# Kernel optimization log

Hardware: AMD Instinct MI355X
Metric: run time of the kernel (lower is better)

The kernel has to match this reference:

```python
import jax, jax.numpy as jnp
import numpy as np

N_NODES = 100000
N_EDGES = 800000
IN_DIM, HID_DIM, OUT_DIM = 128, 64, 7


def setup_inputs() -> dict:
    key = jax.random.key(0)
    ks = jax.random.split(key, 8)
    x = jax.random.normal(ks[0], (N_NODES, IN_DIM), dtype=jnp.float32)
    edge_index = jax.random.randint(ks[1], (2, N_EDGES), 0, N_NODES, dtype=jnp.int64)
    # Glorot-ish init for weights, zeros for bias (PyG GCNConv default)
    def glorot(k, shape):
        lim = float(np.sqrt(6.0 / (shape[0] + shape[1])))
        return jax.random.uniform(k, shape, dtype=jnp.float32, minval=-lim, maxval=lim)
    return {
        "x": x,
        "edge_index": edge_index,
        "W1": glorot(ks[2], (IN_DIM, HID_DIM)),
        "b1": jnp.zeros((HID_DIM,), jnp.float32),
        "W2": glorot(ks[3], (HID_DIM, HID_DIM)),
        "b2": jnp.zeros((HID_DIM,), jnp.float32),
        "W3": glorot(ks[4], (HID_DIM, OUT_DIM)),
        "b3": jnp.zeros((OUT_DIM,), jnp.float32),
    }


def _gcn_conv(h_in, src, dst, W, b, n_nodes):
    # PyG GCNConv: h = x @ W; add self-loops; D^-1/2 A_hat D^-1/2 aggregation; + b
    h = h_in @ W  # [N, F_out]
    # degree over destination nodes, +1 for self-loop
    deg = jax.ops.segment_sum(jnp.ones_like(dst, dtype=h.dtype), dst,
                              num_segments=n_nodes) + 1.0
    dinv = jax.lax.rsqrt(deg)  # [N]
    coef = dinv[src] * dinv[dst]  # [E]
    msg = h[src] * coef[:, None]  # gather + scale  [E, F_out]
    out = jax.ops.segment_sum(msg, dst, num_segments=n_nodes)  # scatter-add
    out = out + h * (dinv * dinv)[:, None]  # self-loop contribution
    return out + b


def reference(x, edge_index, W1, b1, W2, b2, W3, b3):
    src, dst = edge_index[0], edge_index[1]
    n = x.shape[0]
    h = jax.nn.relu(_gcn_conv(x, src, dst, W1, b1, n))
    # dropout(p=0.5) is identity in eval mode
    h = jax.nn.relu(_gcn_conv(h, src, dst, W2, b2, n))
    return _gcn_conv(h, src, dst, W3, b3, n)
```

## Files before the change

kernel.cpp:

```cpp
#include <hip/hip_runtime.h>

#define N_NODES 100000
#define N_EDGES 800000
#define IN_DIM 128
#define HID 64
#define OUT_DIM 7
#define CAP 32
#define NGROUP 4
#define DSLICE (N_NODES / NGROUP)
#define SUBBLK 780
#define NB_N ((N_NODES + 255) / 256)

typedef __bf16 vbf8 __attribute__((ext_vector_type(8)));
typedef float  vf4  __attribute__((ext_vector_type(4)));

__device__ __forceinline__ void wswz_body(int idx, const float* __restrict__ W,
                                          __bf16* __restrict__ out) {
    int j  = idx & 7;
    int l  = (idx >> 3) & 63;
    int nt = (idx >> 9) & 3;
    int ks = idx >> 11;
    int k  = ks * 32 + ((l >> 4) << 3) + j;
    int n  = nt * 16 + (l & 15);
    out[idx] = (__bf16)W[k * 64 + n];
}

__global__ __launch_bounds__(256)
void k_init(const float* __restrict__ W1, __bf16* __restrict__ Wz1,
            const float* __restrict__ W2, __bf16* __restrict__ Wz2) {
    int b = blockIdx.x;
    if (b < 32) wswz_body(b * 256 + threadIdx.x, W1, Wz1);
    else        wswz_body((b - 32) * 256 + threadIdx.x, W2, Wz2);
}

template<int K, bool F32IN>
__device__ __forceinline__ void gemm_mfma_body(int g, int tid,
                                               const void* __restrict__ Xv,
                                               const __bf16* __restrict__ Wswz,
                                               __bf16* __restrict__ Hb) {
    constexpr int KS = K / 32;
    const int lane = tid & 63;
    const int w = g * 4 + (tid >> 6);
    if (w >= N_NODES / 16) return;
    const int r0 = w * 16;
    const int m = lane & 15;
    const int quad = lane >> 4;

    vbf8 bfrag[KS][4];
    const vbf8* wp = (const vbf8*)Wswz;
    #pragma unroll
    for (int ks = 0; ks < KS; ++ks)
        #pragma unroll
        for (int nt = 0; nt < 4; ++nt)
            bfrag[ks][nt] = wp[(ks * 4 + nt) * 64 + lane];

    vf4 acc[4] = {};
    #pragma unroll
    for (int ks = 0; ks < KS; ++ks) {
        vbf8 a;
        if (F32IN) {
            const float* xp = (const float*)Xv + (size_t)(r0 + m) * K + ks * 32 + quad * 8;
            float4 f0 = *(const float4*)xp;
            float4 f1 = *(const float4*)(xp + 4);
            a[0] = (__bf16)f0.x; a[1] = (__bf16)f0.y; a[2] = (__bf16)f0.z; a[3] = (__bf16)f0.w;
            a[4] = (__bf16)f1.x; a[5] = (__bf16)f1.y; a[6] = (__bf16)f1.z; a[7] = (__bf16)f1.w;
        } else {
            a = *(const vbf8*)((const __bf16*)Xv + (size_t)(r0 + m) * K + ks * 32 + quad * 8);
        }
        #pragma unroll
        for (int nt = 0; nt < 4; ++nt)
            acc[nt] = __builtin_amdgcn_mfma_f32_16x16x32_bf16(a, bfrag[ks][nt], acc[nt], 0, 0, 0);
    }
    #pragma unroll
    for (int nt = 0; nt < 4; ++nt)
        #pragma unroll
        for (int r = 0; r < 4; ++r)
            Hb[(size_t)(r0 + quad * 4 + r) * 64 + nt * 16 + m] = (__bf16)acc[nt][r];
}

#define FILL_BLKS (NGROUP * SUBBLK)
#define GEMM_BLKS ((N_NODES / 16 + 3) / 4)
__global__ __launch_bounds__(256)
void k_build_gemm1(const int* __restrict__ ei, int* __restrict__ cnt,
                   int* __restrict__ csr, const float* __restrict__ X,
                   const __bf16* __restrict__ Wz1, __bf16* __restrict__ Hb) {
    int b = blockIdx.x;
    if (b < GEMM_BLKS) {
        gemm_mfma_body<IN_DIM, true>(b, threadIdx.x, X, Wz1, Hb);
    } else {
        int bb = b - GEMM_BLKS;
        int group = bb & 3, sub = bb >> 2;
        int lo = group * DSLICE;
        const int4* dst4 = (const int4*)(ei + N_EDGES);
        const int4* src4 = (const int4*)ei;
        for (int e4 = sub * 256 + threadIdx.x; e4 < N_EDGES / 4; e4 += SUBBLK * 256) {
            int4 d4 = dst4[e4];
            int4 s4 = src4[e4];
            bool m0 = (unsigned)(d4.x - lo) < (unsigned)DSLICE;
            bool m1 = (unsigned)(d4.y - lo) < (unsigned)DSLICE;
            bool m2 = (unsigned)(d4.z - lo) < (unsigned)DSLICE;
            bool m3 = (unsigned)(d4.w - lo) < (unsigned)DSLICE;
            if (!(m0 | m1 | m2 | m3)) continue;
            if (m0) { int p = atomicAdd(&cnt[d4.x], 1); if (p < CAP) csr[(size_t)d4.x * CAP + p] = s4.x; }
            if (m1) { int p = atomicAdd(&cnt[d4.y], 1); if (p < CAP) csr[(size_t)d4.y * CAP + p] = s4.y; }
            if (m2) { int p = atomicAdd(&cnt[d4.z], 1); if (p < CAP) csr[(size_t)d4.z * CAP + p] = s4.z; }
            if (m3) { int p = atomicAdd(&cnt[d4.w], 1); if (p < CAP) csr[(size_t)d4.w * CAP + p] = s4.w; }
        }
    }
}

__global__ __launch_bounds__(256)
void k_gemm2(const __bf16* __restrict__ Ab, const __bf16* __restrict__ Wz2,
             __bf16* __restrict__ Hb) {
    gemm_mfma_body<HID, false>(blockIdx.x, threadIdx.x, Ab, Wz2, Hb);
}

__global__ __launch_bounds__(256)
void k_gather64(const int* __restrict__ cnt, const int* __restrict__ csr,
                const float* __restrict__ bias, const __bf16* __restrict__ Hb,
                __bf16* __restrict__ Ab) {
    int node = blockIdx.x * 32 + (threadIdx.x >> 3);
    int q = threadIdx.x & 7;
    if (node >= N_NODES) return;
    int deg = cnt[node];
    int end = deg < CAP ? deg : CAP;
    float dd = rsqrtf((float)deg + 1.0f);
    float d2 = dd * dd;
    vbf8 h8 = *(const vbf8*)(Hb + (size_t)node * 64 + q * 8);
    float4 b0 = *(const float4*)(bias + q * 8);
    float4 b1 = *(const float4*)(bias + q * 8 + 4);
    float acc[8];
    acc[0] = fmaf((float)h8[0], d2, b0.x); acc[1] = fmaf((float)h8[1], d2, b0.y);
    acc[2] = fmaf((float)h8[2], d2, b0.z); acc[3] = fmaf((float)h8[3], d2, b0.w);
    acc[4] = fmaf((float)h8[4], d2, b1.x); acc[5] = fmaf((float)h8[5], d2, b1.y);
    acc[6] = fmaf((float)h8[6], d2, b1.z); acc[7] = fmaf((float)h8[7], d2, b1.w);

    const int4* row4 = (const int4*)(csr + (size_t)node * CAP);
    int4 qa = row4[0], qb = row4[1], qc = row4[2], qd = row4[3];
    int srcs[16] = {qa.x, qa.y, qa.z, qa.w, qb.x, qb.y, qb.z, qb.w,
                    qc.x, qc.y, qc.z, qc.w, qd.x, qd.y, qd.z, qd.w};
    #pragma unroll
    for (int t = 0; t < 16; ++t) {
        bool live = t < end;
        int s = live ? srcs[t] : node;
        int cs = cnt[s];
        vbf8 v = *(const vbf8*)(Hb + (size_t)s * 64 + q * 8);
        float c = live ? rsqrtf((float)cs + 1.0f) * dd : 0.0f;
        #pragma unroll
        for (int u = 0; u < 8; ++u) acc[u] = fmaf((float)v[u], c, acc[u]);
    }
    for (int j = 16; j < end; ++j) {
        int s = (csr + (size_t)node * CAP)[j];
        float c = rsqrtf((float)cnt[s] + 1.0f) * dd;
        vbf8 v = *(const vbf8*)(Hb + (size_t)s * 64 + q * 8);
        #pragma unroll
        for (int u = 0; u < 8; ++u) acc[u] = fmaf((float)v[u], c, acc[u]);
    }
    vbf8 o;
    #pragma unroll
    for (int t = 0; t < 8; ++t) o[t] = (__bf16)fmaxf(acc[t], 0.f);
    *(vbf8*)(Ab + (size_t)node * 64 + q * 8) = o;
}

__global__ __launch_bounds__(256)
void k_gather64m(const int* __restrict__ cnt, const int* __restrict__ csr,
                 const float* __restrict__ bias, const __bf16* __restrict__ Hb,
                 const float* __restrict__ W3, float* __restrict__ S) {
    int node = blockIdx.x * 32 + (threadIdx.x >> 3);
    int q = threadIdx.x & 7;
    if (node >= N_NODES) return;
    int deg = cnt[node];
    int end = deg < CAP ? deg : CAP;
    float dd = rsqrtf((float)deg + 1.0f);
    float d2 = dd * dd;
    vbf8 h8 = *(const vbf8*)(Hb + (size_t)node * 64 + q * 8);
    float4 b0 = *(const float4*)(bias + q * 8);
    float4 b1 = *(const float4*)(bias + q * 8 + 4);
    float acc[8];
    acc[0] = fmaf((float)h8[0], d2, b0.x); acc[1] = fmaf((float)h8[1], d2, b0.y);
    acc[2] = fmaf((float)h8[2], d2, b0.z); acc[3] = fmaf((float)h8[3], d2, b0.w);
    acc[4] = fmaf((float)h8[4], d2, b1.x); acc[5] = fmaf((float)h8[5], d2, b1.y);
    acc[6] = fmaf((float)h8[6], d2, b1.z); acc[7] = fmaf((float)h8[7], d2, b1.w);

    const int4* row4 = (const int4*)(csr + (size_t)node * CAP);
    int4 qa = row4[0], qb = row4[1], qc = row4[2], qd = row4[3];
    int srcs[16] = {qa.x, qa.y, qa.z, qa.w, qb.x, qb.y, qb.z, qb.w,
                    qc.x, qc.y, qc.z, qc.w, qd.x, qd.y, qd.z, qd.w};
    #pragma unroll
    for (int t = 0; t < 16; ++t) {
        bool live = t < end;
        int s = live ? srcs[t] : node;
        int cs = cnt[s];
        vbf8 v = *(const vbf8*)(Hb + (size_t)s * 64 + q * 8);
        float c = live ? rsqrtf((float)cs + 1.0f) * dd : 0.0f;
        #pragma unroll
        for (int u = 0; u < 8; ++u) acc[u] = fmaf((float)v[u], c, acc[u]);
    }
    for (int j = 16; j < end; ++j) {
        int s = (csr + (size_t)node * CAP)[j];
        float c = rsqrtf((float)cnt[s] + 1.0f) * dd;
        vbf8 v = *(const vbf8*)(Hb + (size_t)s * 64 + q * 8);
        #pragma unroll
        for (int u = 0; u < 8; ++u) acc[u] = fmaf((float)v[u], c, acc[u]);
    }

    float p[7] = {};
    #pragma unroll
    for (int t = 0; t < 8; ++t) {
        float r = fmaxf(acc[t], 0.f);
        #pragma unroll
        for (int j = 0; j < 7; ++j)
            p[j] = fmaf(r, W3[(q * 8 + t) * 7 + j], p[j]);
    }
    #pragma unroll
    for (int msk = 1; msk < 8; msk <<= 1)
        #pragma unroll
        for (int j = 0; j < 7; ++j)
            p[j] += __shfl_xor(p[j], msk, 8);
    if (q < 7) {
        float v = p[0];
        if (q == 1) v = p[1]; else if (q == 2) v = p[2]; else if (q == 3) v = p[3];
        else if (q == 4) v = p[4]; else if (q == 5) v = p[5]; else if (q == 6) v = p[6];
        S[(size_t)node * 7 + q] = v;
    }
}

__global__ __launch_bounds__(256)
void k_gather7(const int* __restrict__ cnt, const int* __restrict__ csr,
               const float* __restrict__ S, const float* __restrict__ b3,
               float* __restrict__ Out) {
    int node = blockIdx.x * 32 + (threadIdx.x >> 3);
    int j7 = threadIdx.x & 7;
    if (node >= N_NODES || j7 >= 7) return;
    int deg = cnt[node];
    int end = deg < CAP ? deg : CAP;
    float dd = rsqrtf((float)deg + 1.0f);
    float d2 = dd * dd;
    const int4* row4 = (const int4*)(csr + (size_t)node * CAP);
    int4 qa = row4[0], qb = row4[1], qc = row4[2], qd = row4[3];
    int srcs[16] = {qa.x, qa.y, qa.z, qa.w, qb.x, qb.y, qb.z, qb.w,
                    qc.x, qc.y, qc.z, qc.w, qd.x, qd.y, qd.z, qd.w};
    float acc = fmaf(S[(size_t)node * 7 + j7], d2, b3[j7]);
    #pragma unroll
    for (int t = 0; t < 16; ++t) {
        bool live = t < end;
        int s = live ? srcs[t] : node;
        int cs = cnt[s];
        float v = S[(size_t)s * 7 + j7];
        float c = live ? rsqrtf((float)cs + 1.0f) * dd : 0.0f;
        acc = fmaf(v, c, acc);
    }
    for (int j = 16; j < end; ++j) {
        int s = (csr + (size_t)node * CAP)[j];
        float c = rsqrtf((float)cnt[s] + 1.0f) * dd;
        acc = fmaf(S[(size_t)s * 7 + j7], c, acc);
    }
    Out[(size_t)node * 7 + j7] = acc;
}

static inline size_t align256(size_t x) { return (x + 255) & ~(size_t)255; }

extern "C" void kernel_launch(void* const* d_in, const int* in_sizes, int n_in,
                              void* d_out, int out_size, void* d_ws, size_t ws_size,
                              hipStream_t stream) {
    const float* x  = (const float*)d_in[0];
    const int*   ei = (const int*)d_in[1];
    const float* W1 = (const float*)d_in[2];
    const float* b1 = (const float*)d_in[3];
    const float* W2 = (const float*)d_in[4];
    const float* b2 = (const float*)d_in[5];
    const float* W3 = (const float*)d_in[6];
    const float* b3 = (const float*)d_in[7];
    float* out = (float*)d_out;

    char* wsp = (char*)d_ws;
    int*    cnt  = (int*)wsp;    wsp += align256(sizeof(int) * N_NODES);
    int*    csr  = (int*)wsp;    wsp += align256(sizeof(int) * (size_t)N_NODES * CAP);
    __bf16* Wz1  = (__bf16*)wsp; wsp += align256(sizeof(__bf16) * IN_DIM * 64);
    __bf16* Wz2  = (__bf16*)wsp; wsp += align256(sizeof(__bf16) * HID * 64);
    __bf16* HbA  = (__bf16*)wsp; wsp += align256(sizeof(__bf16) * (size_t)N_NODES * 64);
    __bf16* Ab   = (__bf16*)wsp; wsp += align256(sizeof(__bf16) * (size_t)N_NODES * 64);
    __bf16* HbB  = (__bf16*)wsp; wsp += align256(sizeof(__bf16) * (size_t)N_NODES * 64);
    float*  bufS = (float*)wsp;  wsp += align256(sizeof(float) * (size_t)N_NODES * 7);

    hipMemsetAsync(cnt, 0, sizeof(int) * N_NODES, stream);
    k_init<<<48, 256, 0, stream>>>(W1, Wz1, W2, Wz2);
    k_build_gemm1<<<GEMM_BLKS + FILL_BLKS, 256, 0, stream>>>(ei, cnt, csr, x, Wz1, HbA);
    k_gather64<<<N_NODES / 32, 256, 0, stream>>>(cnt, csr, b1, HbA, Ab);
    k_gemm2<<<GEMM_BLKS, 256, 0, stream>>>(Ab, Wz2, HbB);
    k_gather64m<<<N_NODES / 32, 256, 0, stream>>>(cnt, csr, b2, HbB, W3, bufS);
    k_gather7<<<N_NODES / 32, 256, 0, stream>>>(cnt, csr, bufS, b3, out);
}
```

Before: 231.3 us.

## Pre-scale features by source degree and use zero sentinel row in gathers

Factors the symmetric normalization so each node's features are pre-multiplied by its own dinv (a new scale kernel after GEMM1, folded into the GEMM2 epilogue, and applied to the layer-3 S output). Gathers then just sum neighbour rows and apply the destination dinv and bias once. This removes per-edge cnt lookups and rsqrt. Inactive slots read a zeroed sentinel row N_NODES instead of being masked. The CSR build also splits the edge scan into 8 destination slices instead of 4, and an extra elementwise pass over H1 is added.

```diff
diff --git a/kernel.cpp b/kernel.cpp
--- a/kernel.cpp
+++ b/kernel.cpp
@@ -6,9 +6,9 @@
 #define HID 64
 #define OUT_DIM 7
 #define CAP 32
-#define NGROUP 4
+#define NGROUP 8
 #define DSLICE (N_NODES / NGROUP)
-#define SUBBLK 780
+#define SUBBLK 390
 #define NB_N ((N_NODES + 255) / 256)
 
 typedef __bf16 vbf8 __attribute__((ext_vector_type(8)));
@@ -27,18 +27,22 @@
 
 __global__ __launch_bounds__(256)
 void k_init(const float* __restrict__ W1, __bf16* __restrict__ Wz1,
-            const float* __restrict__ W2, __bf16* __restrict__ Wz2) {
+            const float* __restrict__ W2, __bf16* __restrict__ Wz2,
+            __bf16* __restrict__ HbA, __bf16* __restrict__ HbB,
+            float* __restrict__ S) {
     int b = blockIdx.x;
-    if (b < 32) wswz_body(b * 256 + threadIdx.x, W1, Wz1);
-    else        wswz_body((b - 32) * 256 + threadIdx.x, W2, Wz2);
-}
-
-template<int K, bool F32IN>
-__device__ __forceinline__ void gemm_mfma_body(int g, int tid,
-                                               const void* __restrict__ Xv,
-                                               const __bf16* __restrict__ Wswz,
-                                               __bf16* __restrict__ Hb) {
-    constexpr int KS = K / 32;
+    int t = threadIdx.x;
+    if (b < 32) { wswz_body(b * 256 + t, W1, Wz1); return; }
+    if (b < 48) { wswz_body((b - 32) * 256 + t, W2, Wz2); return; }
+    if (t < 32)       ((unsigned*)(HbA + (size_t)N_NODES * 64))[t] = 0u;
+    else if (t < 64)  ((unsigned*)(HbB + (size_t)N_NODES * 64))[t - 32] = 0u;
+    else if (t < 71)  S[(size_t)N_NODES * 7 + (t - 64)] = 0.0f;
+}
+
+__device__ __forceinline__ void gemm1_body(int g, int tid, const float* __restrict__ X,
+                                           const __bf16* __restrict__ Wswz,
+                                           __bf16* __restrict__ Hb) {
+    constexpr int K = IN_DIM, KS = K / 32;
     const int lane = tid & 63;
     const int w = g * 4 + (tid >> 6);
     if (w >= N_NODES / 16) return;
@@ -57,16 +61,12 @@
     vf4 acc[4] = {};
     #pragma unroll
     for (int ks = 0; ks < KS; ++ks) {
+        const float* xp = X + (size_t)(r0 + m) * K + ks * 32 + quad * 8;
+        float4 f0 = *(const float4*)xp;
+        float4 f1 = *(const float4*)(xp + 4);
         vbf8 a;
-        if (F32IN) {
-            const float* xp = (const float*)Xv + (size_t)(r0 + m) * K + ks * 32 + quad * 8;
-            float4 f0 = *(const float4*)xp;
-            float4 f1 = *(const float4*)(xp + 4);
-            a[0] = (__bf16)f0.x; a[1] = (__bf16)f0.y; a[2] = (__bf16)f0.z; a[3] = (__bf16)f0.w;
-            a[4] = (__bf16)f1.x; a[5] = (__bf16)f1.y; a[6] = (__bf16)f1.z; a[7] = (__bf16)f1.w;
-        } else {
-            a = *(const vbf8*)((const __bf16*)Xv + (size_t)(r0 + m) * K + ks * 32 + quad * 8);
-        }
+        a[0] = (__bf16)f0.x; a[1] = (__bf16)f0.y; a[2] = (__bf16)f0.z; a[3] = (__bf16)f0.w;
+        a[4] = (__bf16)f1.x; a[5] = (__bf16)f1.y; a[6] = (__bf16)f1.z; a[7] = (__bf16)f1.w;
         #pragma unroll
         for (int nt = 0; nt < 4; ++nt)
             acc[nt] = __builtin_amdgcn_mfma_f32_16x16x32_bf16(a, bfrag[ks][nt], acc[nt], 0, 0, 0);
@@ -86,10 +86,10 @@
                    const __bf16* __restrict__ Wz1, __bf16* __restrict__ Hb) {
     int b = blockIdx.x;
     if (b < GEMM_BLKS) {
-        gemm_mfma_body<IN_DIM, true>(b, threadIdx.x, X, Wz1, Hb);
+        gemm1_body(b, threadIdx.x, X, Wz1, Hb);
     } else {
         int bb = b - GEMM_BLKS;
-        int group = bb & 3, sub = bb >> 2;
+        int group = bb & 7, sub = bb >> 3;
         int lo = group * DSLICE;
         const int4* dst4 = (const int4*)(ei + N_EDGES);
         const int4* src4 = (const int4*)ei;
@@ -110,14 +110,58 @@
 }
 
 __global__ __launch_bounds__(256)
+void k_scale(const int* __restrict__ cnt, __bf16* __restrict__ Hb) {
+    int idx = (blockIdx.x * 256 + threadIdx.x) * 8;
+    int row = idx >> 6;
+    float dinv = rsqrtf((float)cnt[row] + 1.0f);
+    vbf8 v = *(const vbf8*)(Hb + idx);
+    #pragma unroll
+    for (int t = 0; t < 8; ++t) v[t] = (__bf16)((float)v[t] * dinv);
+    *(vbf8*)(Hb + idx) = v;
+}
+
+__global__ __launch_bounds__(256)
 void k_gemm2(const __bf16* __restrict__ Ab, const __bf16* __restrict__ Wz2,
-             __bf16* __restrict__ Hb) {
-    gemm_mfma_body<HID, false>(blockIdx.x, threadIdx.x, Ab, Wz2, Hb);
+             const int* __restrict__ cnt, __bf16* __restrict__ Hb) {
+    constexpr int KS = 2;
+    const int tid = threadIdx.x;
+    const int lane = tid & 63;
+    const int w = blockIdx.x * 4 + (tid >> 6);
+    if (w >= N_NODES / 16) return;
+    const int r0 = w * 16;
+    const int m = lane & 15;
+    const int quad = lane >> 4;
+
+    vbf8 bfrag[KS][4];
+    const vbf8* wp = (const vbf8*)Wz2;
+    #pragma unroll
+    for (int ks = 0; ks < KS; ++ks)
+        #pragma unroll
+        for (int nt = 0; nt < 4; ++nt)
+            bfrag[ks][nt] = wp[(ks * 4 + nt) * 64 + lane];
+
+    vf4 acc[4] = {};
+    #pragma unroll
+    for (int ks = 0; ks < KS; ++ks) {
+        vbf8 a = *(const vbf8*)(Ab + (size_t)(r0 + m) * 64 + ks * 32 + quad * 8);
+        #pragma unroll
+        for (int nt = 0; nt < 4; ++nt)
+            acc[nt] = __builtin_amdgcn_mfma_f32_16x16x32_bf16(a, bfrag[ks][nt], acc[nt], 0, 0, 0);
+    }
+    float dv[4];
+    #pragma unroll
+    for (int r = 0; r < 4; ++r)
+        dv[r] = rsqrtf((float)cnt[r0 + quad * 4 + r] + 1.0f);
+    #pragma unroll
+    for (int nt = 0; nt < 4; ++nt)
+        #pragma unroll
+        for (int r = 0; r < 4; ++r)
+            Hb[(size_t)(r0 + quad * 4 + r) * 64 + nt * 16 + m] = (__bf16)(acc[nt][r] * dv[r]);
 }
 
 __global__ __launch_bounds__(256)
 void k_gather64(const int* __restrict__ cnt, const int* __restrict__ csr,
-                const float* __restrict__ bias, const __bf16* __restrict__ Hb,
+                const float* __restrict__ bias, const __bf16* __restrict__ Hs,
                 __bf16* __restrict__ Ab) {
     int node = blockIdx.x * 32 + (threadIdx.x >> 3);
     int q = threadIdx.x & 7;
@@ -125,15 +169,10 @@
     int deg = cnt[node];
     int end = deg < CAP ? deg : CAP;
     float dd = rsqrtf((float)deg + 1.0f);
-    float d2 = dd * dd;
-    vbf8 h8 = *(const vbf8*)(Hb + (size_t)node * 64 + q * 8);
-    float4 b0 = *(const float4*)(bias + q * 8);
-    float4 b1 = *(const float4*)(bias + q * 8 + 4);
+    vbf8 h8 = *(const vbf8*)(Hs + (size_t)node * 64 + q * 8);
     float acc[8];
-    acc[0] = fmaf((float)h8[0], d2, b0.x); acc[1] = fmaf((float)h8[1], d2, b0.y);
-    acc[2] = fmaf((float)h8[2], d2, b0.z); acc[3] = fmaf((float)h8[3], d2, b0.w);
-    acc[4] = fmaf((float)h8[4], d2, b1.x); acc[5] = fmaf((float)h8[5], d2, b1.y);
-    acc[6] = fmaf((float)h8[6], d2, b1.z); acc[7] = fmaf((float)h8[7], d2, b1.w);
+    #pragma unroll
+    for (int t = 0; t < 8; ++t) acc[t] = (float)h8[t];
 
     const int4* row4 = (const int4*)(csr + (size_t)node * CAP);
     int4 qa = row4[0], qb = row4[1], qc = row4[2], qd = row4[3];
@@ -141,30 +180,29 @@
                     qc.x, qc.y, qc.z, qc.w, qd.x, qd.y, qd.z, qd.w};
     #pragma unroll
     for (int t = 0; t < 16; ++t) {
-        bool live = t < end;
-        int s = live ? srcs[t] : node;
-        int cs = cnt[s];
-        vbf8 v = *(const vbf8*)(Hb + (size_t)s * 64 + q * 8);
-        float c = live ? rsqrtf((float)cs + 1.0f) * dd : 0.0f;
-        #pragma unroll
-        for (int u = 0; u < 8; ++u) acc[u] = fmaf((float)v[u], c, acc[u]);
+        int s = (t < end) ? srcs[t] : N_NODES;
+        vbf8 v = *(const vbf8*)(Hs + (size_t)s * 64 + q * 8);
+        #pragma unroll
+        for (int u = 0; u < 8; ++u) acc[u] += (float)v[u];
     }
     for (int j = 16; j < end; ++j) {
         int s = (csr + (size_t)node * CAP)[j];
-        float c = rsqrtf((float)cnt[s] + 1.0f) * dd;
-        vbf8 v = *(const vbf8*)(Hb + (size_t)s * 64 + q * 8);
-        #pragma unroll
-        for (int u = 0; u < 8; ++u) acc[u] = fmaf((float)v[u], c, acc[u]);
-    }
+        vbf8 v = *(const vbf8*)(Hs + (size_t)s * 64 + q * 8);
+        #pragma unroll
+        for (int u = 0; u < 8; ++u) acc[u] += (float)v[u];
+    }
+    float4 b0 = *(const float4*)(bias + q * 8);
+    float4 b1 = *(const float4*)(bias + q * 8 + 4);
+    float bb[8] = {b0.x, b0.y, b0.z, b0.w, b1.x, b1.y, b1.z, b1.w};
     vbf8 o;
     #pragma unroll
-    for (int t = 0; t < 8; ++t) o[t] = (__bf16)fmaxf(acc[t], 0.f);
+    for (int t = 0; t < 8; ++t) o[t] = (__bf16)fmaxf(fmaf(acc[t], dd, bb[t]), 0.f);
     *(vbf8*)(Ab + (size_t)node * 64 + q * 8) = o;
 }
 
 __global__ __launch_bounds__(256)
 void k_gather64m(const int* __restrict__ cnt, const int* __restrict__ csr,
-                 const float* __restrict__ bias, const __bf16* __restrict__ Hb,
+                 const float* __restrict__ bias, const __bf16* __restrict__ Hs,
                  const float* __restrict__ W3, float* __restrict__ S) {
     int node = blockIdx.x * 32 + (threadIdx.x >> 3);
     int q = threadIdx.x & 7;
@@ -172,15 +210,10 @@
     int deg = cnt[node];
     int end = deg < CAP ? deg : CAP;
     float dd = rsqrtf((float)deg + 1.0f);
-    float d2 = dd * dd;
-    vbf8 h8 = *(const vbf8*)(Hb + (size_t)node * 64 + q * 8);
-    float4 b0 = *(const float4*)(bias + q * 8);
-    float4 b1 = *(const float4*)(bias + q * 8 + 4);
+    vbf8 h8 = *(const vbf8*)(Hs + (size_t)node * 64 + q * 8);
     float acc[8];
-    acc[0] = fmaf((float)h8[0], d2, b0.x); acc[1] = fmaf((float)h8[1], d2, b0.y);
-    acc[2] = fmaf((float)h8[2], d2, b0.z); acc[3] = fmaf((float)h8[3], d2, b0.w);
-    acc[4] = fmaf((float)h8[4], d2, b1.x); acc[5] = fmaf((float)h8[5], d2, b1.y);
-    acc[6] = fmaf((float)h8[6], d2, b1.z); acc[7] = fmaf((float)h8[7], d2, b1.w);
+    #pragma unroll
+    for (int t = 0; t < 8; ++t) acc[t] = (float)h8[t];
 
     const int4* row4 = (const int4*)(csr + (size_t)node * CAP);
     int4 qa = row4[0], qb = row4[1], qc = row4[2], qd = row4[3];
@@ -188,26 +221,25 @@
                     qc.x, qc.y, qc.z, qc.w, qd.x, qd.y, qd.z, qd.w};
     #pragma unroll
     for (int t = 0; t < 16; ++t) {
-        bool live = t < end;
-        int s = live ? srcs[t] : node;
-        int cs = cnt[s];
-        vbf8 v = *(const vbf8*)(Hb + (size_t)s * 64 + q * 8);
-        float c = live ? rsqrtf((float)cs + 1.0f) * dd : 0.0f;
-        #pragma unroll
-        for (int u = 0; u < 8; ++u) acc[u] = fmaf((float)v[u], c, acc[u]);
+        int s = (t < end) ? srcs[t] : N_NODES;
+        vbf8 v = *(const vbf8*)(Hs + (size_t)s * 64 + q * 8);
+        #pragma unroll
+        for (int u = 0; u < 8; ++u) acc[u] += (float)v[u];
     }
     for (int j = 16; j < end; ++j) {
         int s = (csr + (size_t)node * CAP)[j];
-        float c = rsqrtf((float)cnt[s] + 1.0f) * dd;
-        vbf8 v = *(const vbf8*)(Hb + (size_t)s * 64 + q * 8);
-        #pragma unroll
-        for (int u = 0; u < 8; ++u) acc[u] = fmaf((float)v[u], c, acc[u]);
-    }
-
+        vbf8 v = *(const vbf8*)(Hs + (size_t)s * 64 + q * 8);
+        #pragma unroll
+        for (int u = 0; u < 8; ++u) acc[u] += (float)v[u];
+    }
+
+    float4 b0 = *(const float4*)(bias + q * 8);
+    float4 b1 = *(const float4*)(bias + q * 8 + 4);
+    float bb[8] = {b0.x, b0.y, b0.z, b0.w, b1.x, b1.y, b1.z, b1.w};
     float p[7] = {};
     #pragma unroll
     for (int t = 0; t < 8; ++t) {
-        float r = fmaxf(acc[t], 0.f);
+        float r = fmaxf(fmaf(acc[t], dd, bb[t]), 0.f);
         #pragma unroll
         for (int j = 0; j < 7; ++j)
             p[j] = fmaf(r, W3[(q * 8 + t) * 7 + j], p[j]);
@@ -221,7 +253,7 @@
         float v = p[0];
         if (q == 1) v = p[1]; else if (q == 2) v = p[2]; else if (q == 3) v = p[3];
         else if (q == 4) v = p[4]; else if (q == 5) v = p[5]; else if (q == 6) v = p[6];
-        S[(size_t)node * 7 + q] = v;
+        S[(size_t)node * 7 + q] = v * dd;
     }
 }
 
@@ -235,27 +267,21 @@
     int deg = cnt[node];
     int end = deg < CAP ? deg : CAP;
     float dd = rsqrtf((float)deg + 1.0f);
-    float d2 = dd * dd;
     const int4* row4 = (const int4*)(csr + (size_t)node * CAP);
     int4 qa = row4[0], qb = row4[1], qc = row4[2], qd = row4[3];
     int srcs[16] = {qa.x, qa.y, qa.z, qa.w, qb.x, qb.y, qb.z, qb.w,
                     qc.x, qc.y, qc.z, qc.w, qd.x, qd.y, qd.z, qd.w};
-    float acc = fmaf(S[(size_t)node * 7 + j7], d2, b3[j7]);
+    float acc = S[(size_t)node * 7 + j7];
     #pragma unroll
     for (int t = 0; t < 16; ++t) {
-        bool live = t < end;
-        int s = live ? srcs[t] : node;
-        int cs = cnt[s];
-        float v = S[(size_t)s * 7 + j7];
-        float c = live ? rsqrtf((float)cs + 1.0f) * dd : 0.0f;
-        acc = fmaf(v, c, acc);
+        int s = (t < end) ? srcs[t] : N_NODES;
+        acc += S[(size_t)s * 7 + j7];
     }
     for (int j = 16; j < end; ++j) {
         int s = (csr + (size_t)node * CAP)[j];
-        float c = rsqrtf((float)cnt[s] + 1.0f) * dd;
-        acc = fmaf(S[(size_t)s * 7 + j7], c, acc);
-    }
-    Out[(size_t)node * 7 + j7] = acc;
+        acc += S[(size_t)s * 7 + j7];
+    }
+    Out[(size_t)node * 7 + j7] = fmaf(acc, dd, b3[j7]);
 }
 
 static inline size_t align256(size_t x) { return (x + 255) & ~(size_t)255; }
@@ -278,16 +304,17 @@
     int*    csr  = (int*)wsp;    wsp += align256(sizeof(int) * (size_t)N_NODES * CAP);
     __bf16* Wz1  = (__bf16*)wsp; wsp += align256(sizeof(__bf16) * IN_DIM * 64);
     __bf16* Wz2  = (__bf16*)wsp; wsp += align256(sizeof(__bf16) * HID * 64);
-    __bf16* HbA  = (__bf16*)wsp; wsp += align256(sizeof(__bf16) * (size_t)N_NODES * 64);
+    __bf16* HbA  = (__bf16*)wsp; wsp += align256(sizeof(__bf16) * (size_t)(N_NODES + 1) * 64);
     __bf16* Ab   = (__bf16*)wsp; wsp += align256(sizeof(__bf16) * (size_t)N_NODES * 64);
-    __bf16* HbB  = (__bf16*)wsp; wsp += align256(sizeof(__bf16) * (size_t)N_NODES * 64);
-    float*  bufS = (float*)wsp;  wsp += align256(sizeof(float) * (size_t)N_NODES * 7);
+    __bf16* HbB  = (__bf16*)wsp; wsp += align256(sizeof(__bf16) * (size_t)(N_NODES + 1) * 64);
+    float*  bufS = (float*)wsp;  wsp += align256(sizeof(float) * (size_t)(N_NODES + 1) * 7);
 
     hipMemsetAsync(cnt, 0, sizeof(int) * N_NODES, stream);
-    k_init<<<48, 256, 0, stream>>>(W1, Wz1, W2, Wz2);
+    k_init<<<49, 256, 0, stream>>>(W1, Wz1, W2, Wz2, HbA, HbB, bufS);
     k_build_gemm1<<<GEMM_BLKS + FILL_BLKS, 256, 0, stream>>>(ei, cnt, csr, x, Wz1, HbA);
+    k_scale<<<(N_NODES * 64) / (8 * 256), 256, 0, stream>>>(cnt, HbA);
     k_gather64<<<N_NODES / 32, 256, 0, stream>>>(cnt, csr, b1, HbA, Ab);
-    k_gemm2<<<GEMM_BLKS, 256, 0, stream>>>(Ab, Wz2, HbB);
+    k_gemm2<<<GEMM_BLKS, 256, 0, stream>>>(Ab, Wz2, cnt, HbB);
     k_gather64m<<<N_NODES / 32, 256, 0, stream>>>(cnt, csr, b2, HbB, W3, bufS);
     k_gather7<<<N_NODES / 32, 256, 0, stream>>>(cnt, csr, bufS, b3, out);
 }
```

After: 204.4 us. 11.7% less time.
